# Optimization experiments

Measured on AMD Instinct MI355X. Metric: run time of the kernel, lower is better.

Reference implementation:

```python
import jax, jax.numpy as jnp
import numpy as np

B, T, P, V, D, DINO, H, L = 32, 40, 256, 4096, 256, 384, 4, 2
HD = D // H          # head dim 64
DFF = 4 * D          # 1024
EPS = 1e-5


def setup_inputs() -> dict:
    key = jax.random.key(0)
    ks = iter(jax.random.split(key, 40))
    rn = lambda shape, s=0.02: jax.random.normal(next(ks), shape, jnp.float32) * s
    return dict(
        patches=jax.random.normal(next(ks), (B, P, DINO), jnp.float32),
        tokens=jax.random.randint(next(ks), (B, T), 0, V, jnp.int32),
        tok_emb=rn((V, D)),
        pos_emb=rn((1, T, D)),
        qkv_w=rn((L, 3 * D, D)), qkv_b=jnp.zeros((L, 3 * D), jnp.float32),
        out_w=rn((L, D, D)), out_b=jnp.zeros((L, D), jnp.float32),
        ln1_s=jnp.ones((L, D), jnp.float32), ln1_b=jnp.zeros((L, D), jnp.float32),
        w1=rn((L, DFF, D)), b1=jnp.zeros((L, DFF), jnp.float32),
        w2=rn((L, D, DFF)), b2=jnp.zeros((L, D), jnp.float32),
        ln2_s=jnp.ones((L, D), jnp.float32), ln2_b=jnp.zeros((L, D), jnp.float32),
        fus_w1=rn((D, DINO + D)), fus_b1=jnp.zeros((D,), jnp.float32),
        fus_w2=rn((D, D)), fus_b2=jnp.zeros((D,), jnp.float32),
        cls_w=rn((V, D)), cls_b=jnp.zeros((V,), jnp.float32),
    )


def _ln(x, s, b):
    m = jnp.mean(x, -1, keepdims=True)
    v = jnp.var(x, -1, keepdims=True)
    return (x - m) * jax.lax.rsqrt(v + EPS) * s + b


def _token_encoder(tokens, tok_emb, pos_emb, qkv_w, qkv_b, out_w, out_b,
                   ln1_s, ln1_b, w1, b1, w2, b2, ln2_s, ln2_b):
    # Causal full-sequence pass: output at position t equals re-running the
    # unmasked encoder on tokens[:, :t+1] and taking the last position.
    x = tok_emb[tokens] + pos_emb[:, :tokens.shape[1], :]   # [B,T,D]
    causal = jnp.triu(jnp.full((T, T), -1e9, jnp.float32), 1)  # [T,T]
    for l in range(L):  # fixed small layer count
        qkv = x @ qkv_w[l].T + qkv_b[l]                     # [B,T,3D]
        q, k, v = jnp.split(qkv, 3, axis=-1)
        q = q.reshape(B, T, H, HD).transpose(0, 2, 1, 3)    # [B,H,T,hd]
        k = k.reshape(B, T, H, HD).transpose(0, 2, 1, 3)
        v = v.reshape(B, T, H, HD).transpose(0, 2, 1, 3)
        scores = jnp.einsum('bhqd,bhkd->bhqk', q, k) / np.sqrt(HD).astype(np.float32)
        attn = jax.nn.softmax(scores + causal, axis=-1)
        ctx = jnp.einsum('bhqk,bhkd->bhqd', attn, v)        # [B,H,T,hd]
        ctx = ctx.transpose(0, 2, 1, 3).reshape(B, T, D)
        x = _ln(x + ctx @ out_w[l].T + out_b[l], ln1_s[l], ln1_b[l])
        h = jax.nn.relu(x @ w1[l].T + b1[l]) @ w2[l].T + b2[l]
        x = _ln(x + h, ln2_s[l], ln2_b[l])
    return x  # [B,T,D]


def reference(patches, tokens, tok_emb, pos_emb, qkv_w, qkv_b, out_w, out_b,
              ln1_s, ln1_b, w1, b1, w2, b2, ln2_s, ln2_b,
              fus_w1, fus_b1, fus_w2, fus_b2, cls_w, cls_b):
    enc = _token_encoder(tokens, tok_emb, pos_emb, qkv_w, qkv_b, out_w, out_b,
                         ln1_s, ln1_b, w1, b1, w2, b2, ln2_s, ln2_b)  # [B,T,D]
    # context for step 0 is zeros; step t>0 uses encoder output at position t-1
    ctx = jnp.concatenate([jnp.zeros((B, 1, D), enc.dtype), enc[:, :-1]], axis=1)  # [B,T,D]
    # fusion MLP: split the concat-linear into a patch part and a context part
    wp, wc = fus_w1[:, :DINO], fus_w1[:, DINO:]
    pproj = patches @ wp.T                                  # [B,P,D]
    cproj = ctx @ wc.T + fus_b1                             # [B,T,D]
    h = jax.nn.gelu(pproj[:, None, :, :] + cproj[:, :, None, :], approximate=False)  # [B,T,P,D]
    fused = h @ fus_w2.T + fus_b2                           # [B,T,P,D]
    # sigmoid+gather of the 4096-way logits == gather classifier rows, dot, sigmoid
    w_sel = cls_w[tokens]                                   # [B,T,D]
    b_sel = cls_b[tokens]                                   # [B,T]
    logits = jnp.einsum('btpd,btd->btp', fused, w_sel) + b_sel[:, :, None]
    probs = jax.nn.sigmoid(logits)                          # [B,T,P]
    return probs.transpose(0, 2, 1)                         # [B,P,T] == [B,256,40]
```

## Files before the change

kernel.cpp:

```cpp
#include <hip/hip_runtime.h>
#include <hip/hip_bf16.h>

#define B_ 32
#define T_ 40
#define P_ 256
#define V_ 4096
#define D_ 256
#define DINO_ 384
#define H_ 4
#define L_ 2
#define HD_ 64
#define DFF_ 1024
#define EPS_ 1e-5f

typedef __bf16 bf16;
typedef __bf16 bf16x8 __attribute__((ext_vector_type(8)));
typedef float f32x4 __attribute__((ext_vector_type(4)));

#define OFF_QKV 0
#define OFF_OUTW 393216
#define OFF_W1 524288
#define OFF_W2 1048576
#define OFF_FUS 1572864
#define WB_TOTAL 1736704
#define CONV_BLOCKS 848
#define PAT_BLOCKS 1536

__device__ __forceinline__ bf16x8 cvt8(const float* p) {
  float4 f0 = *(const float4*)p;
  float4 f1 = *(const float4*)(p + 4);
  bf16x8 v;
  v[0] = (bf16)f0.x; v[1] = (bf16)f0.y; v[2] = (bf16)f0.z; v[3] = (bf16)f0.w;
  v[4] = (bf16)f1.x; v[5] = (bf16)f1.y; v[6] = (bf16)f1.z; v[7] = (bf16)f1.w;
  return v;
}

__global__ __launch_bounds__(256) void prep_k(
    const int* __restrict__ tokens, const float* __restrict__ tok_emb,
    const float* __restrict__ pos_emb, float* __restrict__ x,
    const float* __restrict__ fus_w2, bf16* __restrict__ w2Tb,
    const float* __restrict__ qkv_w, const float* __restrict__ out_w,
    const float* __restrict__ w1, const float* __restrict__ w2,
    const float* __restrict__ fus_w1, bf16* __restrict__ wb,
    const float* __restrict__ patches, bf16* __restrict__ patb) {
  __shared__ float tile[32][33];
  int bi = blockIdx.x;
  int tid = threadIdx.x;
  if (bi < B_ * T_) {
    int t = bi % T_;
    x[bi * D_ + tid] = tok_emb[tokens[bi] * D_ + tid] + pos_emb[t * D_ + tid];
  } else if (bi < B_ * T_ + 64) {
    int tt = bi - B_ * T_;
    int bx = (tt & 7) * 32, by = (tt >> 3) * 32;
    int tx = tid & 31, ty = tid >> 5;
#pragma unroll
    for (int i = 0; i < 32; i += 8) tile[ty + i][tx] = fus_w2[(by + ty + i) * D_ + bx + tx];
    __syncthreads();
#pragma unroll
    for (int i = 0; i < 32; i += 8)
      w2Tb[(bx + ty + i) * D_ + by + tx] = (bf16)tile[tx][ty + i];
  } else if (bi < B_ * T_ + 64 + CONV_BLOCKS) {
    long f = (long)(bi - B_ * T_ - 64) * 2048 + tid * 8;
    const float* src;
    long off;
    if (f < OFF_OUTW)      { src = qkv_w;  off = f - OFF_QKV; }
    else if (f < OFF_W1)   { src = out_w;  off = f - OFF_OUTW; }
    else if (f < OFF_W2)   { src = w1;     off = f - OFF_W1; }
    else if (f < OFF_FUS)  { src = w2;     off = f - OFF_W2; }
    else                   { src = fus_w1; off = f - OFF_FUS; }
    *(bf16x8*)&wb[f] = cvt8(src + off);
  } else {
    long f = (long)(bi - B_ * T_ - 64 - CONV_BLOCKS) * 2048 + tid * 8;
    *(bf16x8*)&patb[f] = cvt8(patches + f);
  }
}

template <int ABF16, int OBF16, int RELU, int RESID>
__global__ __launch_bounds__(256) void gemm_k(
    const void* __restrict__ Av, const bf16* __restrict__ W,
    const float* __restrict__ bias, const float* __restrict__ resid,
    void* __restrict__ outv, int K, int lda, int ldw, int ldc) {
  __shared__ bf16 As[32 * 72];
  __shared__ bf16 Ws[32 * 72];
  const int tid = threadIdx.x;
  const int lane = tid & 63;
  const int wv = tid >> 6;
  const int mi = wv & 1, ni = wv >> 1;
  const int col = lane & 15, quad = lane >> 4;
  const int bn = blockIdx.x * 32, bm = blockIdx.y * 32;
  const int srow = tid >> 3, kc = (tid & 7) * 8;
  const float* Af = (const float*)Av;
  const bf16* Ab = (const bf16*)Av;
  const bf16* Wp = W + (long)(bn + srow) * ldw + kc;

  f32x4 acc = {0.f, 0.f, 0.f, 0.f};
  for (int kk = 0; kk < K; kk += 64) {
    if (ABF16)
      *(bf16x8*)&As[srow * 72 + kc] = *(const bf16x8*)(Ab + (long)(bm + srow) * lda + kk + kc);
    else
      *(bf16x8*)&As[srow * 72 + kc] = cvt8(Af + (long)(bm + srow) * lda + kk + kc);
    *(bf16x8*)&Ws[srow * 72 + kc] = *(const bf16x8*)(Wp + kk);
    __syncthreads();
#pragma unroll
    for (int ki = 0; ki < 2; ++ki) {
      bf16x8 afr = *(const bf16x8*)&As[(mi * 16 + col) * 72 + ki * 32 + quad * 8];
      bf16x8 bfr = *(const bf16x8*)&Ws[(ni * 16 + col) * 72 + ki * 32 + quad * 8];
      acc = __builtin_amdgcn_mfma_f32_16x16x32_bf16(afr, bfr, acc, 0, 0, 0);
    }
    __syncthreads();
  }
  const int n = bn + ni * 16 + col;
  float bv = bias ? bias[n] : 0.0f;
#pragma unroll
  for (int r = 0; r < 4; ++r) {
    int m = bm + mi * 16 + quad * 4 + r;
    float val = acc[r] + bv;
    if (RESID) val += resid[(long)m * D_ + n];
    if (RELU) val = fmaxf(val, 0.0f);
    if (OBF16) ((bf16*)outv)[(long)m * ldc + n] = (bf16)val;
    else ((float*)outv)[(long)m * ldc + n] = val;
  }
}

__global__ __launch_bounds__(256) void ln_k(const float* __restrict__ s,
                                            float* __restrict__ xout,
                                            const float* __restrict__ g,
                                            const float* __restrict__ be) {
  int wv = threadIdx.x >> 6, lane = threadIdx.x & 63;
  int m = blockIdx.x * 4 + wv;
  float4 v = *(const float4*)(s + (long)m * D_ + lane * 4);
  float sum = v.x + v.y + v.z + v.w;
  float ss = v.x * v.x + v.y * v.y + v.z * v.z + v.w * v.w;
#pragma unroll
  for (int mk = 1; mk < 64; mk <<= 1) {
    sum += __shfl_xor(sum, mk);
    ss += __shfl_xor(ss, mk);
  }
  float mean = sum * (1.0f / D_);
  float inv = rsqrtf(ss * (1.0f / D_) - mean * mean + EPS_);
  float4 g4 = *(const float4*)(g + lane * 4);
  float4 b4 = *(const float4*)(be + lane * 4);
  float4 o;
  o.x = (v.x - mean) * inv * g4.x + b4.x;
  o.y = (v.y - mean) * inv * g4.y + b4.y;
  o.z = (v.z - mean) * inv * g4.z + b4.z;
  o.w = (v.w - mean) * inv * g4.w + b4.w;
  *(float4*)(xout + (long)m * D_ + lane * 4) = o;
}

__global__ __launch_bounds__(256) void attn_k(const float* __restrict__ qkv,
                                              float* __restrict__ ctx) {
  __shared__ float q[20][HD_ + 1];
  __shared__ float k[T_][HD_ + 1];
  __shared__ float v[T_][HD_ + 1];
  __shared__ float s[20][T_ + 1];
  int h = blockIdx.x, b = blockIdx.y, zq = blockIdx.z;
  int r0 = zq * 20;
  int tid = threadIdx.x;
  for (int idx = tid; idx < T_ * HD_; idx += 256) {
    int t = idx >> 6, d = idx & 63;
    long base = (long)(b * T_ + t) * (3 * D_) + h * HD_ + d;
    k[t][d] = qkv[base + D_];
    v[t][d] = qkv[base + 2 * D_];
    if (t < 20) q[t][d] = qkv[(long)(b * T_ + r0 + t) * (3 * D_) + h * HD_ + d];
  }
  __syncthreads();
  for (int idx = tid; idx < 20 * T_; idx += 256) {
    int i = idx / T_, j = idx - i * T_;
    if (j <= r0 + i) {
      float acc = 0.f;
#pragma unroll
      for (int d = 0; d < HD_; ++d) acc += q[i][d] * k[j][d];
      s[i][j] = acc * 0.125f;
    }
  }
  __syncthreads();
  if (tid < 20) {
    int i = tid, hi = r0 + i;
    float mx = -1e30f;
    for (int j = 0; j <= hi; ++j) mx = fmaxf(mx, s[i][j]);
    float sum = 0.f;
    for (int j = 0; j <= hi; ++j) {
      float e = __expf(s[i][j] - mx);
      s[i][j] = e;
      sum += e;
    }
    float inv = 1.0f / sum;
    for (int j = 0; j <= hi; ++j) s[i][j] *= inv;
  }
  __syncthreads();
  for (int idx = tid; idx < 20 * HD_; idx += 256) {
    int i = idx >> 6, d = idx & 63;
    int hi = r0 + i;
    float acc = 0.f;
    for (int j = 0; j <= hi; ++j) acc += s[i][j] * v[j][d];
    ctx[(long)(b * T_ + hi) * D_ + h * HD_ + d] = acc;
  }
}

__global__ __launch_bounds__(256) void fuse3_k(
    const bf16* __restrict__ patb, const float* __restrict__ xbuf,
    const float* __restrict__ cls_w, const bf16* __restrict__ fusb,
    const bf16* __restrict__ w2Tb, const float* __restrict__ fus_b1,
    const int* __restrict__ tokens, float* __restrict__ pprojT,
    float* __restrict__ cw) {
  __shared__ bf16 As[32 * 72];
  __shared__ bf16 Ws[32 * 72];
  const int tid = threadIdx.x;
  const int lane = tid & 63;
  const int wv = tid >> 6;
  const int mi = wv & 1, ni = wv >> 1;
  const int col = lane & 15, quad = lane >> 4;
  const int bn = blockIdx.x * 32;
  const int y = blockIdx.y;
  const int srow = tid >> 3, kc = (tid & 7) * 8;

  int job, bm, bb = 0;
  if (y < 256) { job = 0; bb = y >> 3; bm = (y & 7) * 32; }
  else if (y < 296) { job = 1; bm = (y - 256) * 32; }
  else { job = 2; bm = (y - 296) * 32; }
  const int gm = bm + srow;

  int K = D_;
  bool zeroA = false;
  const float* Apf = nullptr;
  const bf16* Apb = nullptr;
  const bf16* Wp;
  if (job == 0) {
    Apb = fusb + (long)gm * 640;
    Wp = patb + ((long)bb * P_ + bn + srow) * DINO_ + kc;
    K = DINO_;
  } else if (job == 1) {
    int t = gm % T_;
    zeroA = (t == 0);
    Apf = xbuf + (long)(zeroA ? gm : gm - 1) * D_;
    Wp = fusb + 384 + (long)(bn + srow) * 640 + kc;
  } else {
    Apf = cls_w + (long)tokens[gm] * D_;
    Wp = w2Tb + (long)(bn + srow) * D_ + kc;
  }

  f32x4 acc = {0.f, 0.f, 0.f, 0.f};
  bf16x8 z8 = {};
  for (int kk = 0; kk < K; kk += 64) {
    bf16x8 av;
    if (job == 0) av = *(const bf16x8*)(Apb + kk + kc);
    else if (zeroA) av = z8;
    else av = cvt8(Apf + kk + kc);
    *(bf16x8*)&As[srow * 72 + kc] = av;
    *(bf16x8*)&Ws[srow * 72 + kc] = *(const bf16x8*)(Wp + kk);
    __syncthreads();
#pragma unroll
    for (int ki = 0; ki < 2; ++ki) {
      bf16x8 afr = *(const bf16x8*)&As[(mi * 16 + col) * 72 + ki * 32 + quad * 8];
      bf16x8 bfr = *(const bf16x8*)&Ws[(ni * 16 + col) * 72 + ki * 32 + quad * 8];
      acc = __builtin_amdgcn_mfma_f32_16x16x32_bf16(afr, bfr, acc, 0, 0, 0);
    }
    __syncthreads();
  }
  const int n = bn + ni * 16 + col;
  if (job == 0) {
#pragma unroll
    for (int r4 = 0; r4 < 4; ++r4) {
      int e = bm + mi * 16 + quad * 4 + r4;
      pprojT[(long)bb * (D_ * P_) + (long)e * P_ + n] = acc[r4];
    }
  } else if (job == 1) {
    float bv = fus_b1[n];
#pragma unroll
    for (int r4 = 0; r4 < 4; ++r4) {
      int m = bm + mi * 16 + quad * 4 + r4;
      cw[(long)m * (2 * D_) + n * 2] = acc[r4] + bv;
    }
  } else {
#pragma unroll
    for (int r4 = 0; r4 < 4; ++r4) {
      int m = bm + mi * 16 + quad * 4 + r4;
      cw[(long)m * (2 * D_) + n * 2 + 1] = acc[r4];
    }
  }
}

__global__ __launch_bounds__(256) void final_k(const float* __restrict__ pprojT,
                                               const float* __restrict__ cw,
                                               const int* __restrict__ tokens,
                                               const float* __restrict__ cls_w,
                                               const float* __restrict__ cls_b,
                                               const float* __restrict__ fus_b2,
                                               float* __restrict__ out) {
  __shared__ float2 cws[4][D_];
  int tid = threadIdx.x;
  int lane = tid & 63, wv = tid >> 6;
  int p = blockIdx.x * 64 + lane;
  int t = blockIdx.y * 4 + wv;
  int b = blockIdx.z;
  int mbase = b * T_ + blockIdx.y * 4;
  for (int idx = tid; idx < 4 * D_; idx += 256) {
    int tt = idx >> 8, e = idx & 255;
    cws[tt][e] = ((const float2*)cw)[(long)(mbase + tt) * D_ + e];
  }
  __syncthreads();

  int m = b * T_ + t;
  int tok = tokens[m];
  const float* cr = cls_w + (long)tok * D_;
  float bacc = 0.f;
#pragma unroll
  for (int i = 0; i < 4; ++i) bacc += cr[lane + i * 64] * fus_b2[lane + i * 64];
#pragma unroll
  for (int mk = 1; mk < 64; mk <<= 1) bacc += __shfl_xor(bacc, mk);
  float beff = bacc + cls_b[tok];

  const float* ppb = pprojT + (long)b * (D_ * P_);
  float acc = 0.f;
#pragma unroll 8
  for (int e = 0; e < D_; ++e) {
    float pp = ppb[e * P_ + p];
    float2 c = cws[wv][e];
    float x = pp + c.x;
    float x2 = x * x;
    float u = x * fmaf(-0.1029432f, x2, -2.3022083f);
    float ex = __builtin_amdgcn_exp2f(u);
    float r = __builtin_amdgcn_rcpf(1.0f + ex);
    acc = fmaf(x * r, c.y, acc);
  }
  float logit = acc + beff;
  float es = __builtin_amdgcn_exp2f(-1.4426950408889634f * logit);
  out[(long)(b * P_ + p) * T_ + t] = __builtin_amdgcn_rcpf(1.0f + es);
}

extern "C" void kernel_launch(void* const* d_in, const int* in_sizes, int n_in, void* d_out,
                              int out_size, void* d_ws, size_t ws_size, hipStream_t stream) {
  const float* patches = (const float*)d_in[0];
  const int* tokens = (const int*)d_in[1];
  const float* tok_emb = (const float*)d_in[2];
  const float* pos_emb = (const float*)d_in[3];
  const float* qkv_w = (const float*)d_in[4];
  const float* qkv_b = (const float*)d_in[5];
  const float* out_w = (const float*)d_in[6];
  const float* out_b = (const float*)d_in[7];
  const float* ln1_s = (const float*)d_in[8];
  const float* ln1_b = (const float*)d_in[9];
  const float* w1 = (const float*)d_in[10];
  const float* b1 = (const float*)d_in[11];
  const float* w2 = (const float*)d_in[12];
  const float* b2 = (const float*)d_in[13];
  const float* ln2_s = (const float*)d_in[14];
  const float* ln2_b = (const float*)d_in[15];
  const float* fus_w1 = (const float*)d_in[16];
  const float* fus_b1 = (const float*)d_in[17];
  const float* fus_w2 = (const float*)d_in[18];
  const float* fus_b2 = (const float*)d_in[19];
  const float* cls_w = (const float*)d_in[20];
  const float* cls_b = (const float*)d_in[21];
  float* out = (float*)d_out;

  const int MT = B_ * T_;
  float* x = (float*)d_ws;
  float* qkvbuf = x + MT * D_;
  float* attbuf = qkvbuf + MT * 3 * D_;
  float* s = attbuf + MT * D_;
  float* pprojT = s + MT * D_;
  float* cwbuf = pprojT + (long)B_ * D_ * P_;
  bf16* wb = (bf16*)(cwbuf + MT * D_ * 2);
  bf16* w2Tb = wb + WB_TOTAL;
  bf16* patb = w2Tb + D_ * D_;
  bf16* hb = patb + (long)B_ * P_ * DINO_;

  prep_k<<<MT + 64 + CONV_BLOCKS + PAT_BLOCKS, 256, 0, stream>>>(
      tokens, tok_emb, pos_emb, x, fus_w2, w2Tb, qkv_w, out_w, w1, w2, fus_w1, wb,
      patches, patb);

  for (int l = 0; l < L_; ++l) {
    gemm_k<0, 0, 0, 0><<<dim3(24, 40), 256, 0, stream>>>(
        x, wb + OFF_QKV + (long)l * 3 * D_ * D_, qkv_b + l * 3 * D_, nullptr, qkvbuf,
        D_, D_, D_, 3 * D_);
    attn_k<<<dim3(H_, B_, 2), 256, 0, stream>>>(qkvbuf, attbuf);
    gemm_k<0, 0, 0, 1><<<dim3(8, 40), 256, 0, stream>>>(
        attbuf, wb + OFF_OUTW + (long)l * D_ * D_, out_b + l * D_, x, s, D_, D_, D_, D_);
    ln_k<<<MT / 4, 256, 0, stream>>>(s, x, ln1_s + l * D_, ln1_b + l * D_);
    gemm_k<0, 1, 1, 0><<<dim3(32, 40), 256, 0, stream>>>(
        x, wb + OFF_W1 + (long)l * DFF_ * D_, b1 + l * DFF_, nullptr, hb, D_, D_, D_, DFF_);
    gemm_k<1, 0, 0, 1><<<dim3(8, 40), 256, 0, stream>>>(
        hb, wb + OFF_W2 + (long)l * D_ * DFF_, b2 + l * D_, x, s, DFF_, DFF_, DFF_, D_);
    ln_k<<<MT / 4, 256, 0, stream>>>(s, x, ln2_s + l * D_, ln2_b + l * D_);
  }

  fuse3_k<<<dim3(8, 336), 256, 0, stream>>>(patb, x, cls_w, wb + OFF_FUS, w2Tb,
                                            fus_b1, tokens, pprojT, cwbuf);

  final_k<<<dim3(4, 10, 32), 256, 0, stream>>>(pprojT, cwbuf, tokens, cls_w, cls_b,
                                               fus_b2, out);
}
```

Measured before the change: 251.7 us.

## Fuse final layernorm into fusion GEMM, parallelize softmax, cheapen GELU approximation

The serial per-row softmax in the attention kernel becomes a wave-parallel version that uses shuffle reductions for the max and the sum. The last layer's second layernorm is dropped from the layer loop and computed inside fuse3_k's context-projection job. That job stages a full normalized 32x256 bf16 A tile in shared memory, which removes one kernel launch and one round trip of the activations. In final_k, the tanh-style GELU polynomial is replaced by the cheaper x*sigmoid(1.702x) form. That form is a looser approximation of exact GELU and may push the output closer to the accuracy tolerance.

```diff
diff --git a/kernel.cpp b/kernel.cpp
--- a/kernel.cpp
+++ b/kernel.cpp
@@ -157,6 +157,7 @@
   int h = blockIdx.x, b = blockIdx.y, zq = blockIdx.z;
   int r0 = zq * 20;
   int tid = threadIdx.x;
+  int lane = tid & 63, wv = tid >> 6;
   for (int idx = tid; idx < T_ * HD_; idx += 256) {
     int t = idx >> 6, d = idx & 63;
     long base = (long)(b * T_ + t) * (3 * D_) + h * HD_ + d;
@@ -175,18 +176,20 @@
     }
   }
   __syncthreads();
-  if (tid < 20) {
-    int i = tid, hi = r0 + i;
-    float mx = -1e30f;
-    for (int j = 0; j <= hi; ++j) mx = fmaxf(mx, s[i][j]);
-    float sum = 0.f;
-    for (int j = 0; j <= hi; ++j) {
-      float e = __expf(s[i][j] - mx);
-      s[i][j] = e;
-      sum += e;
-    }
-    float inv = 1.0f / sum;
-    for (int j = 0; j <= hi; ++j) s[i][j] *= inv;
+  for (int rr = wv; rr < 20; rr += 4) {
+    int hi = r0 + rr;
+    float val = (lane <= hi) ? s[rr][lane] : -1e30f;
+    float mx = val;
+#pragma unroll
+    for (int mk = 1; mk < 64; mk <<= 1) mx = fmaxf(mx, __shfl_xor(mx, mk));
+    float e = (lane <= hi)
+                  ? __builtin_amdgcn_exp2f((val - mx) * 1.4426950408889634f)
+                  : 0.f;
+    float sum = e;
+#pragma unroll
+    for (int mk = 1; mk < 64; mk <<= 1) sum += __shfl_xor(sum, mk);
+    float inv = __builtin_amdgcn_rcpf(sum);
+    if (lane < T_) s[rr][lane] = e * inv;
   }
   __syncthreads();
   for (int idx = tid; idx < 20 * HD_; idx += 256) {
@@ -199,12 +202,13 @@
 }
 
 __global__ __launch_bounds__(256) void fuse3_k(
-    const bf16* __restrict__ patb, const float* __restrict__ xbuf,
+    const bf16* __restrict__ patb, const float* __restrict__ sbuf,
+    const float* __restrict__ lng, const float* __restrict__ lnb,
     const float* __restrict__ cls_w, const bf16* __restrict__ fusb,
     const bf16* __restrict__ w2Tb, const float* __restrict__ fus_b1,
     const int* __restrict__ tokens, float* __restrict__ pprojT,
     float* __restrict__ cw) {
-  __shared__ bf16 As[32 * 72];
+  __shared__ bf16 As[32 * 264];
   __shared__ bf16 Ws[32 * 72];
   const int tid = threadIdx.x;
   const int lane = tid & 63;
@@ -221,43 +225,90 @@
   else { job = 2; bm = (y - 296) * 32; }
   const int gm = bm + srow;
 
-  int K = D_;
-  bool zeroA = false;
-  const float* Apf = nullptr;
-  const bf16* Apb = nullptr;
-  const bf16* Wp;
-  if (job == 0) {
-    Apb = fusb + (long)gm * 640;
-    Wp = patb + ((long)bb * P_ + bn + srow) * DINO_ + kc;
-    K = DINO_;
-  } else if (job == 1) {
-    int t = gm % T_;
-    zeroA = (t == 0);
-    Apf = xbuf + (long)(zeroA ? gm : gm - 1) * D_;
-    Wp = fusb + 384 + (long)(bn + srow) * 640 + kc;
-  } else {
-    Apf = cls_w + (long)tokens[gm] * D_;
-    Wp = w2Tb + (long)(bn + srow) * D_ + kc;
-  }
-
   f32x4 acc = {0.f, 0.f, 0.f, 0.f};
   bf16x8 z8 = {};
-  for (int kk = 0; kk < K; kk += 64) {
-    bf16x8 av;
-    if (job == 0) av = *(const bf16x8*)(Apb + kk + kc);
-    else if (zeroA) av = z8;
-    else av = cvt8(Apf + kk + kc);
-    *(bf16x8*)&As[srow * 72 + kc] = av;
-    *(bf16x8*)&Ws[srow * 72 + kc] = *(const bf16x8*)(Wp + kk);
+
+  if (job == 1) {
+    const int r = srow, cg = (tid & 7) * 32;
+    const int t = gm % T_;
+    if (t == 0) {
+#pragma unroll
+      for (int i = 0; i < 4; ++i) *(bf16x8*)&As[r * 264 + cg + i * 8] = z8;
+    } else {
+      const float* sp = sbuf + (long)(gm - 1) * D_ + cg;
+      float v[32];
+      float sum = 0.f, ss = 0.f;
+#pragma unroll
+      for (int i = 0; i < 8; ++i) {
+        float4 f = *(const float4*)(sp + i * 4);
+        v[i*4] = f.x; v[i*4+1] = f.y; v[i*4+2] = f.z; v[i*4+3] = f.w;
+        sum += f.x + f.y + f.z + f.w;
+        ss += f.x*f.x + f.y*f.y + f.z*f.z + f.w*f.w;
+      }
+#pragma unroll
+      for (int mk = 1; mk < 8; mk <<= 1) {
+        sum += __shfl_xor(sum, mk);
+        ss += __shfl_xor(ss, mk);
+      }
+      float mean = sum * (1.0f / D_);
+      float inv = rsqrtf(ss * (1.0f / D_) - mean * mean + EPS_);
+#pragma unroll
+      for (int i = 0; i < 8; ++i) {
+        float4 g4 = *(const float4*)(lng + cg + i * 4);
+        float4 b4 = *(const float4*)(lnb + cg + i * 4);
+        As[r*264 + cg + i*4]     = (bf16)((v[i*4]   - mean) * inv * g4.x + b4.x);
+        As[r*264 + cg + i*4 + 1] = (bf16)((v[i*4+1] - mean) * inv * g4.y + b4.y);
+        As[r*264 + cg + i*4 + 2] = (bf16)((v[i*4+2] - mean) * inv * g4.z + b4.z);
+        As[r*264 + cg + i*4 + 3] = (bf16)((v[i*4+3] - mean) * inv * g4.w + b4.w);
+      }
+    }
     __syncthreads();
-#pragma unroll
-    for (int ki = 0; ki < 2; ++ki) {
-      bf16x8 afr = *(const bf16x8*)&As[(mi * 16 + col) * 72 + ki * 32 + quad * 8];
-      bf16x8 bfr = *(const bf16x8*)&Ws[(ni * 16 + col) * 72 + ki * 32 + quad * 8];
-      acc = __builtin_amdgcn_mfma_f32_16x16x32_bf16(afr, bfr, acc, 0, 0, 0);
-    }
-    __syncthreads();
-  }
+    const bf16* Wp = fusb + 384 + (long)(bn + srow) * 640 + kc;
+    for (int kk = 0; kk < 256; kk += 64) {
+      *(bf16x8*)&Ws[srow * 72 + kc] = *(const bf16x8*)(Wp + kk);
+      __syncthreads();
+#pragma unroll
+      for (int ki = 0; ki < 2; ++ki) {
+        bf16x8 afr = *(const bf16x8*)&As[(mi*16 + col) * 264 + kk + ki*32 + quad*8];
+        bf16x8 bfr = *(const bf16x8*)&Ws[(ni*16 + col) * 72 + ki*32 + quad*8];
+        acc = __builtin_amdgcn_mfma_f32_16x16x32_bf16(afr, bfr, acc, 0, 0, 0);
+      }
+      __syncthreads();
+    }
+  } else {
+    const bf16* Apb;
+    const bf16* Wp;
+    int K;
+    bool gathF = false;
+    const float* Apf = nullptr;
+    if (job == 0) {
+      Apb = fusb + (long)gm * 640;
+      Wp = patb + ((long)bb * P_ + bn + srow) * DINO_ + kc;
+      K = DINO_;
+    } else {
+      gathF = true;
+      Apf = cls_w + (long)tokens[gm] * D_;
+      Wp = w2Tb + (long)(bn + srow) * D_ + kc;
+      K = D_;
+      Apb = nullptr;
+    }
+    for (int kk = 0; kk < K; kk += 64) {
+      bf16x8 av;
+      if (gathF) av = cvt8(Apf + kk + kc);
+      else av = *(const bf16x8*)(Apb + kk + kc);
+      *(bf16x8*)&As[srow * 72 + kc] = av;
+      *(bf16x8*)&Ws[srow * 72 + kc] = *(const bf16x8*)(Wp + kk);
+      __syncthreads();
+#pragma unroll
+      for (int ki = 0; ki < 2; ++ki) {
+        bf16x8 afr = *(const bf16x8*)&As[(mi * 16 + col) * 72 + ki * 32 + quad * 8];
+        bf16x8 bfr = *(const bf16x8*)&Ws[(ni * 16 + col) * 72 + ki * 32 + quad * 8];
+        acc = __builtin_amdgcn_mfma_f32_16x16x32_bf16(afr, bfr, acc, 0, 0, 0);
+      }
+      __syncthreads();
+    }
+  }
+
   const int n = bn + ni * 16 + col;
   if (job == 0) {
 #pragma unroll
@@ -318,9 +369,7 @@
     float pp = ppb[e * P_ + p];
     float2 c = cws[wv][e];
     float x = pp + c.x;
-    float x2 = x * x;
-    float u = x * fmaf(-0.1029432f, x2, -2.3022083f);
-    float ex = __builtin_amdgcn_exp2f(u);
+    float ex = __builtin_amdgcn_exp2f(-2.4554248f * x);
     float r = __builtin_amdgcn_rcpf(1.0f + ex);
     acc = fmaf(x * r, c.y, acc);
   }
@@ -383,11 +432,12 @@
         x, wb + OFF_W1 + (long)l * DFF_ * D_, b1 + l * DFF_, nullptr, hb, D_, D_, D_, DFF_);
     gemm_k<1, 0, 0, 1><<<dim3(8, 40), 256, 0, stream>>>(
         hb, wb + OFF_W2 + (long)l * D_ * DFF_, b2 + l * D_, x, s, DFF_, DFF_, DFF_, D_);
-    ln_k<<<MT / 4, 256, 0, stream>>>(s, x, ln2_s + l * D_, ln2_b + l * D_);
-  }
-
-  fuse3_k<<<dim3(8, 336), 256, 0, stream>>>(patb, x, cls_w, wb + OFF_FUS, w2Tb,
-                                            fus_b1, tokens, pprojT, cwbuf);
+    if (l == 0) ln_k<<<MT / 4, 256, 0, stream>>>(s, x, ln2_s + l * D_, ln2_b + l * D_);
+  }
+
+  fuse3_k<<<dim3(8, 336), 256, 0, stream>>>(patb, s, ln2_s + D_, ln2_b + D_, cls_w,
+                                            wb + OFF_FUS, w2Tb, fus_b1, tokens,
+                                            pprojT, cwbuf);
 
   final_k<<<dim3(4, 10, 32), 256, 0, stream>>>(pprojT, cwbuf, tokens, cls_w, cls_b,
                                                fus_b2, out);
```

After: 244.4 us. 2.9% less time.
